# Kernel optimization log

Measured on AMD Instinct MI355X. Metric: run time of the kernel, lower is better.

The kernel has to match this reference:

```python
import jax, jax.numpy as jnp
import numpy as np

V, H, L, BW = 32000, 512, 2, 5   # vocab, hidden(=embed), gru layers, beam width
NEG = -1e9                        # -inf surrogate for duplicate initial beams


def gru_cell(x, h, Wi, Wh, bi, bh):
    # PyTorch GRU gate order: r, z, n.  x:[B,H] h:[B,H] Wi,Wh:[3H,H]
    gi = x @ Wi.T + bi
    gh = h @ Wh.T + bh
    ir, iz, inn = jnp.split(gi, 3, axis=-1)
    hr, hz, hn = jnp.split(gh, 3, axis=-1)
    r = jax.nn.sigmoid(ir + hr)
    z = jax.nn.sigmoid(iz + hz)
    n = jnp.tanh(inn + r * hn)
    return (1.0 - z) * n + z * h


def setup_inputs() -> dict:
    key = jax.random.key(0)
    ks = jax.random.split(key, 14)
    s = 0.05
    p = lambda k, shape: jax.random.normal(k, shape, jnp.float32) * s
    return {
        "input_seq": jax.random.randint(ks[0], (128, 1), 0, V),
        "input_length": 128,
        "max_length": 64,
        "SOS_token": 1,
        "emb": p(ks[1], (V, H)),
        "enc_Wi": p(ks[2], (L, 3 * H, H)),
        "enc_Wh": p(ks[3], (L, 3 * H, H)),
        "enc_bi": p(ks[4], (L, 3 * H)),
        "enc_bh": p(ks[5], (L, 3 * H)),
        "dec_Wi": p(ks[6], (L, 3 * H, H)),
        "dec_Wh": p(ks[7], (L, 3 * H, H)),
        "dec_bi": p(ks[8], (L, 3 * H)),
        "dec_bh": p(ks[9], (L, 3 * H)),
        "Wc": p(ks[10], (H, 2 * H)),
        "bc": p(ks[11], (H,)),
        "Wout": p(ks[12], (V, H)),
        "bout": p(ks[13], (V,)),
    }


def reference(input_seq, input_length, max_length, SOS_token,
              emb, enc_Wi, enc_Wh, enc_bi, enc_bh,
              dec_Wi, dec_Wh, dec_bi, dec_bh, Wc, bc, Wout, bout):
    # ---- encoder: L-layer GRU over [T,1] token ids ----
    x = emb[input_seq[:, 0]]                    # [T,H]

    def enc_step(h, xt):                        # h:[L,1,H]
        inp = xt[None]                          # [1,H]
        hs = []
        for l in range(L):
            hl = gru_cell(inp, h[l], enc_Wi[l], enc_Wh[l], enc_bi[l], enc_bh[l])
            hs.append(hl)
            inp = hl
        return jnp.stack(hs), inp[0]

    h0 = jnp.zeros((L, 1, H), x.dtype)
    enc_hidden, enc_out = jax.lax.scan(enc_step, h0, x)   # enc_out:[T,H]

    # ---- one decoder step, batched over all BW beams ----
    def dec_step(tokens, hidden):               # tokens:[BW] hidden:[L,BW,H]
        inp = emb[tokens]                       # [BW,H]
        hs = []
        for l in range(L):
            hl = gru_cell(inp, hidden[l], dec_Wi[l], dec_Wh[l], dec_bi[l], dec_bh[l])
            hs.append(hl)
            inp = hl
        rnn = inp                               # [BW,H] top-layer output
        e = jnp.einsum('bh,th->bt', rnn, enc_out)          # Luong dot scores
        a = jax.nn.softmax(e, axis=-1)
        ctx = a @ enc_out                       # [BW,H]
        cc = jnp.tanh(jnp.concatenate([rnn, ctx], axis=-1) @ Wc.T + bc)
        logits = cc @ Wout.T + bout             # [BW,V]
        return logits, jnp.stack(hs)

    # ---- beam search: all beams in one batched decoder call per step ----
    tokens0 = jnp.full((BW,), SOS_token, jnp.int32)
    hid0 = jnp.broadcast_to(enc_hidden, (L, BW, H))
    scores0 = jnp.full((BW,), NEG, jnp.float32).at[0].set(0.0)  # one live beam

    def step(carry, _):
        tokens, hidden, scores = carry
        logits, hidden = dec_step(tokens, hidden)
        logp = jax.nn.log_softmax(logits, axis=-1)
        top_lp, top_idx = jax.lax.top_k(logp, BW)            # [BW,BW]
        cand = (scores[:, None] + top_lp).reshape(-1)        # [BW*BW]
        sc, flat = jax.lax.top_k(cand, BW)
        parent = flat // BW
        new_tok = top_idx.reshape(-1)[flat]
        hidden = hidden[:, parent, :]
        return (new_tok, hidden, sc), (new_tok, parent)

    (_, _, final_scores), (toks, pars) = jax.lax.scan(
        step, (tokens0, hid0, scores0), None, length=max_length)

    # ---- backtrack best hypothesis through parent pointers ----
    best = jnp.argmax(final_scores)

    def back(beam, tp):
        t, p = tp
        return p[beam], t[beam]

    _, seq = jax.lax.scan(back, best, (toks, pars), reverse=True)
    return seq, final_scores[best]
```

## Files before the change

kernel.cpp:

```cpp
#include <hip/hip_runtime.h>
#include <math.h>

#define VV 32000
#define HH 512
#define G3 1536
#define TI 128
#define TO 64
#define NB 5
#define NEGF (-1000000000.0f)
#define NTHR 256
#define NT5 512
#define LSTR 32

struct Params {
  const int* seq;
  const int* sosp;
  const float *emb, *eWi, *eWh, *ebi, *ebh;
  const float *dWi, *dWh, *dbi, *dbh;
  const float *Wc, *bc, *Wout, *bout;
  unsigned* bar;
  int *cur_tok, *toks, *pars, *ptop_i;
  float *gi0, *eout, *h0b, *h1b, *dch, *cc, *ptop_v, *psum, *scores;
  float* out;
};

__device__ __forceinline__ float cldf(const float* p) {
  return __hip_atomic_load(p, __ATOMIC_RELAXED, __HIP_MEMORY_SCOPE_AGENT);
}
__device__ __forceinline__ void cstf(float* p, float v) {
  __hip_atomic_store(p, v, __ATOMIC_RELAXED, __HIP_MEMORY_SCOPE_AGENT);
}
__device__ __forceinline__ int cldi(const int* p) {
  return __hip_atomic_load(p, __ATOMIC_RELAXED, __HIP_MEMORY_SCOPE_AGENT);
}
__device__ __forceinline__ void csti(int* p, int v) {
  __hip_atomic_store(p, v, __ATOMIC_RELAXED, __HIP_MEMORY_SCOPE_AGENT);
}
__device__ __forceinline__ unsigned rldu(const unsigned* p) {
  return __hip_atomic_load(p, __ATOMIC_RELAXED, __HIP_MEMORY_SCOPE_AGENT);
}
typedef unsigned long long u64t;
union F2U { u64t u; float f[2]; };
__device__ __forceinline__ void cld2(float* d, const float* p) {
  F2U x; x.u = __hip_atomic_load((const u64t*)p, __ATOMIC_RELAXED, __HIP_MEMORY_SCOPE_AGENT);
  d[0] = x.f[0]; d[1] = x.f[1];
}

__device__ __forceinline__ void bar_arrive(unsigned* lines, int myline) {
  __syncthreads();
  if (threadIdx.x == 0)
    __hip_atomic_fetch_add(lines + myline * LSTR, 1u,
                           __ATOMIC_RELAXED, __HIP_MEMORY_SCOPE_AGENT);
}
template <int SLP>
__device__ __forceinline__ void bar_wait8(const unsigned* lines, unsigned tgt) {
  if (threadIdx.x < 64) {
    for (;;) {
      unsigned v = tgt;
      if (threadIdx.x < 8) v = rldu(lines + threadIdx.x * LSTR);
      if (__all(v >= tgt)) break;
      __builtin_amdgcn_s_sleep(SLP);
    }
  }
  __syncthreads();
}
__device__ __forceinline__ void bcast_store(unsigned* L, int NL, unsigned tok) {
  asm volatile("s_waitcnt vmcnt(0)" ::: "memory");
  for (int i = 0; i < NL; i++)
    __hip_atomic_store(L + i * LSTR, tok, __ATOMIC_RELAXED, __HIP_MEMORY_SCOPE_AGENT);
}
template <int SLP>
__device__ __forceinline__ void leaf_wait(const unsigned* L, int grp, unsigned tok) {
  if (threadIdx.x == 0) {
    while (rldu(L + grp * LSTR) < tok) __builtin_amdgcn_s_sleep(SLP);
  }
  __syncthreads();
}

__device__ __forceinline__ float wredf(float v) {
#pragma unroll
  for (int o = 32; o; o >>= 1) v += __shfl_xor(v, o, 64);
  return v;
}

__global__ void __launch_bounds__(NTHR) k_e0(Params p) {
  const int wg = blockIdx.x, tid = threadIdx.x;
  const int lane = tid & 63, wv = tid >> 6;
  if (wg == 0) {
    for (int i = tid; i < 2 * HH; i += NTHR) { cstf(&p.h0b[i], 0.f); cstf(&p.h1b[i], 0.f); }
  }
  for (int lr = 0; lr < 6; lr++) {
    int row = wg * 6 + lr;
    const float* W = p.eWi + (size_t)row * HH;
    float w0[8];
#pragma unroll
    for (int j = 0; j < 8; j++) w0[j] = W[j * 64 + lane];
    float bi = p.ebi[row];
    for (int t = wv; t < TI; t += 4) {
      const float* x = p.emb + (size_t)p.seq[t] * HH;
      float s = 0.f;
#pragma unroll
      for (int j = 0; j < 8; j++) s += w0[j] * x[j * 64 + lane];
      s = wredf(s);
      if (lane == 0) p.gi0[(size_t)t * G3 + row] = s + bi;
    }
  }
}

__device__ void enc_step(const Params& p, int T, int wg, int lane, int wv) {
  const int sIn = T & 1, sOut = sIn ^ 1;
  if (wv < 2) {
    if (T < TI) {
      float hv[8];
#pragma unroll
      for (int j = 0; j < 8; j++) hv[j] = cldf(&p.h0b[sIn * HH + j * 64 + lane]);
#pragma unroll
      for (int uu = 0; uu < 4; uu++) {
        int u = wg * 8 + wv * 4 + uu;
        float g[3];
#pragma unroll
        for (int gg = 0; gg < 3; gg++) {
          const float* W = p.eWh + (size_t)(gg * HH + u) * HH;
          float s = 0.f;
#pragma unroll
          for (int j = 0; j < 8; j++) s += W[j * 64 + lane] * hv[j];
          g[gg] = wredf(s);
        }
        if (lane == 0) {
          const float* gr = p.gi0 + (size_t)T * G3;
          float ir = gr[u], iz = gr[HH + u], inn = gr[2 * HH + u];
          float hr = g[0] + p.ebh[u], hz = g[1] + p.ebh[HH + u], hn = g[2] + p.ebh[2 * HH + u];
          float r = 1.f / (1.f + expf(-(ir + hr)));
          float z = 1.f / (1.f + expf(-(iz + hz)));
          float n = tanhf(inn + r * hn);
          float hp = cldf(&p.h0b[sIn * HH + u]);
          cstf(&p.h0b[sOut * HH + u], (1.f - z) * n + z * hp);
        }
      }
    }
  } else {
    if (T >= 1) {
      float xv[8], hv[8];
#pragma unroll
      for (int j = 0; j < 8; j++) {
        xv[j] = cldf(&p.h0b[sIn * HH + j * 64 + lane]);
        hv[j] = cldf(&p.h1b[sOut * HH + j * 64 + lane]);
      }
#pragma unroll
      for (int uu = 0; uu < 4; uu++) {
        int u = wg * 8 + (wv - 2) * 4 + uu;
        float gi[3], gh[3];
#pragma unroll
        for (int gg = 0; gg < 3; gg++) {
          const float* Wi1 = p.eWi + (size_t)G3 * HH + (size_t)(gg * HH + u) * HH;
          const float* Wh1 = p.eWh + (size_t)G3 * HH + (size_t)(gg * HH + u) * HH;
          float si = 0.f, s2 = 0.f;
#pragma unroll
          for (int j = 0; j < 8; j++) { si += Wi1[j * 64 + lane] * xv[j]; s2 += Wh1[j * 64 + lane] * hv[j]; }
          gi[gg] = wredf(si);
          gh[gg] = wredf(s2);
        }
        if (lane == 0) {
          const float* bi = p.ebi + G3;
          const float* bh = p.ebh + G3;
          float ir = gi[0] + bi[u], iz = gi[1] + bi[HH + u], inn = gi[2] + bi[2 * HH + u];
          float hr = gh[0] + bh[u], hz = gh[1] + bh[HH + u], hn = gh[2] + bh[2 * HH + u];
          float r = 1.f / (1.f + expf(-(ir + hr)));
          float z = 1.f / (1.f + expf(-(iz + hz)));
          float n = tanhf(inn + r * hn);
          float hp = cldf(&p.h1b[sOut * HH + u]);
          float hnew = (1.f - z) * n + z * hp;
          cstf(&p.h1b[sIn * HH + u], hnew);
          p.eout[(size_t)(T - 1) * HH + u] = hnew;
        }
      }
    }
  }
}

__global__ void __launch_bounds__(NTHR) k_e1x2(Params p, int k) {
  const int wg = blockIdx.x, tid = threadIdx.x;
  const int lane = tid & 63, wv = tid >> 6;
  unsigned* ceA = p.bar + 0 * LSTR;
  enc_step(p, 2 * k, wg, lane, wv);
  if (2 * k + 1 <= TI) {
    bar_arrive(ceA, wg & 7);
    bar_wait8<2>(ceA, (unsigned)(8 * (k + 1)));
    enc_step(p, 2 * k + 1, wg, lane, wv);
  }
}

__global__ void __launch_bounds__(NTHR) k_d0(Params p) {
  const int wg = blockIdx.x, tid = threadIdx.x;
  for (int i = tid + wg * NTHR; i < 2 * NB * HH; i += 64 * NTHR) {
    int l = i / (NB * HH);
    int rem = i - l * (NB * HH);
    int u = rem % HH;
    p.dch[(size_t)l * NB * HH + rem] = (l == 0) ? cldf(&p.h0b[u]) : cldf(&p.h1b[u]);
  }
  if (wg == 0 && tid < NB) {
    p.cur_tok[tid] = p.sosp[0];
    p.scores[tid] = (tid == 0) ? 0.f : NEGF;
  }
}

template <int LAYER>
__device__ void gru_body(const Params& p, float* sm, int t, int ib, int ob,
                         int wg, int tid, int lane, int wv) {
  float* sx = sm;
  float* sh = sm + NB * HH;
  float* fres = sm + 2 * NB * HH;
  int ct[NB], pr[NB];
#pragma unroll
  for (int b = 0; b < NB; b++) {
    ct[b] = (LAYER == 0) ? cldi(&p.cur_tok[b]) : 0;
    pr[b] = (t == 0) ? b : cldi(&p.pars[(t - 1) * NB + b]);
  }
  for (int i = tid; i < NB * (HH / 2); i += NTHR) {
    int b = i >> 8, c = (i & 255) << 1;
    float x2[2], h2[2];
    if (LAYER == 0) {
      const float* e = p.emb + (size_t)ct[b] * HH + c;
      x2[0] = e[0]; x2[1] = e[1];
    } else {
      cld2(x2, &p.dch[((size_t)(ob * 2 + 0) * NB + b) * HH + c]);
    }
    cld2(h2, &p.dch[((size_t)(ib * 2 + LAYER) * NB + pr[b]) * HH + c]);
    sx[b * HH + c] = x2[0]; sx[b * HH + c + 1] = x2[1];
    sh[b * HH + c] = h2[0]; sh[b * HH + c + 1] = h2[1];
  }
  __syncthreads();
  const float* Wi = p.dWi + (size_t)LAYER * G3 * HH;
  const float* Wh = p.dWh + (size_t)LAYER * G3 * HH;
#pragma unroll
  for (int k = 0; k < 12; k++) {
    const int m_ = k % 6;
    const int f = wv * 12 + k;
    const int ul = f / 6;
    const int u = wg * 8 + ul;
    const float* W = (m_ >= 3 ? Wh : Wi) + (size_t)((m_ % 3) * HH + u) * HH;
    const float* vecb = (m_ >= 3) ? sh : sx;
    float wd[8];
#pragma unroll
    for (int j = 0; j < 8; j++) wd[j] = W[j * 64 + lane];
    float a0 = 0.f, a1 = 0.f, a2 = 0.f, a3 = 0.f, a4 = 0.f;
#pragma unroll
    for (int j = 0; j < 8; j++) {
      float wj = wd[j];
      int o = j * 64 + lane;
      a0 += wj * vecb[0 * HH + o];
      a1 += wj * vecb[1 * HH + o];
      a2 += wj * vecb[2 * HH + o];
      a3 += wj * vecb[3 * HH + o];
      a4 += wj * vecb[4 * HH + o];
    }
    float r0 = wredf(a0), r1 = wredf(a1), r2 = wredf(a2), r3 = wredf(a3), r4 = wredf(a4);
    if (lane == 0) {
      fres[f * NB + 0] = r0; fres[f * NB + 1] = r1; fres[f * NB + 2] = r2;
      fres[f * NB + 3] = r3; fres[f * NB + 4] = r4;
    }
  }
  __syncthreads();
  if (tid < 8 * NB) {
    int ul = tid / NB, b = tid - ul * NB;
    int u = wg * 8 + ul;
    const float* bi = p.dbi + LAYER * G3;
    const float* bh = p.dbh + LAYER * G3;
    float ir = fres[(ul * 6 + 0) * NB + b] + bi[u];
    float iz = fres[(ul * 6 + 1) * NB + b] + bi[HH + u];
    float inn = fres[(ul * 6 + 2) * NB + b] + bi[2 * HH + u];
    float hr = fres[(ul * 6 + 3) * NB + b] + bh[u];
    float hz = fres[(ul * 6 + 4) * NB + b] + bh[HH + u];
    float hn = fres[(ul * 6 + 5) * NB + b] + bh[2 * HH + u];
    float hp = sh[b * HH + u];
    float r = 1.f / (1.f + expf(-(ir + hr)));
    float z = 1.f / (1.f + expf(-(iz + hz)));
    float n = tanhf(inn + r * hn);
    cstf(&p.dch[((size_t)(ob * 2 + LAYER) * NB + b) * HH + u], (1.f - z) * n + z * hp);
  }
  __syncthreads();
}

__global__ void __launch_bounds__(NTHR) k_gru2(Params p, int t) {
  const int wg = blockIdx.x, tid = threadIdx.x;
  const int lane = tid & 63, wv = tid >> 6;
  const int ib = t & 1, ob = ib ^ 1;
  __shared__ float sm[2 * NB * HH + 48 * NB];
  unsigned* gruA = p.bar + 8 * LSTR;
  gru_body<0>(p, sm, t, ib, ob, wg, tid, lane, wv);
  bar_arrive(gruA, wg & 7);
  bar_wait8<2>(gruA, (unsigned)(8 * (t + 1)));
  gru_body<1>(p, sm, t, ib, ob, wg, tid, lane, wv);
}

__global__ void __launch_bounds__(NT5) k_pa56(Params p, int t) {
  const int wg = blockIdx.x, tid = threadIdx.x;
  const int lane = tid & 63, wv = tid >> 6;
  const int ob = (t & 1) ^ 1;
  __shared__ float sm[5760];
  __shared__ unsigned s_mrg;
  unsigned* paA = p.bar + 16 * LSTR;
  unsigned* paF = p.bar + 24 * LSTR;
  unsigned* paL = p.bar + 32 * LSTR;
  unsigned* c5A = p.bar + 48 * LSTR;
  unsigned* c5F = p.bar + 56 * LSTR;

  if (wg < 40) {
    const int b = wg / 8, q = wg % 8;
    float* srnn = sm;
    float* sp = sm + 512;
    float* cpart = sm + 640;
    float* sctx = sm + 4736;
    for (int i = tid; i < HH; i += NT5)
      srnn[i] = cldf(&p.dch[((size_t)(ob * 2 + 1) * NB + b) * HH + i]);
    __syncthreads();
    for (int j = wv; j < TI; j += 8) {
      const float* E = p.eout + (size_t)j * HH;
      float s = 0.f;
#pragma unroll
      for (int k2 = 0; k2 < 8; k2++) s += srnn[k2 * 64 + lane] * E[k2 * 64 + lane];
      s = wredf(s);
      if (lane == 0) sp[j] = s;
    }
    __syncthreads();
    if (wv == 0) {
      float v0 = sp[lane], v1 = sp[64 + lane];
      float mx = fmaxf(v0, v1);
#pragma unroll
      for (int o = 32; o; o >>= 1) mx = fmaxf(mx, __shfl_xor(mx, o, 64));
      float e0 = expf(v0 - mx), e1 = expf(v1 - mx);
      float ss = wredf(e0 + e1);
      sp[lane] = e0 / ss;
      sp[64 + lane] = e1 / ss;
    }
    __syncthreads();
    {
      float cp[8];
#pragma unroll
      for (int k2 = 0; k2 < 8; k2++) cp[k2] = 0.f;
      for (int j = wv; j < TI; j += 8) {
        float spj = sp[j];
        const float* E = p.eout + (size_t)j * HH;
#pragma unroll
        for (int k2 = 0; k2 < 8; k2++) cp[k2] += spj * E[k2 * 64 + lane];
      }
#pragma unroll
      for (int k2 = 0; k2 < 8; k2++) cpart[wv * HH + k2 * 64 + lane] = cp[k2];
    }
    __syncthreads();
    for (int i = tid; i < HH; i += NT5)
      sctx[i] = ((cpart[0 * HH + i] + cpart[1 * HH + i]) + (cpart[2 * HH + i] + cpart[3 * HH + i]))
              + ((cpart[4 * HH + i] + cpart[5 * HH + i]) + (cpart[6 * HH + i] + cpart[7 * HH + i]));
    __syncthreads();
    for (int k = wv; k < 64; k += 8) {
      int u = q * 64 + k;
      const float* W = p.Wc + (size_t)u * (2 * HH);
      float s0 = 0.f, s1 = 0.f;
#pragma unroll
      for (int j = 0; j < 8; j++) {
        int o = j * 64 + lane;
        s0 += W[o] * srnn[o];
        s1 += W[HH + o] * sctx[o];
      }
      float r0 = wredf(s0), r1 = wredf(s1);
      if (lane == 0) cstf(&p.cc[b * HH + u], tanhf(r0 + r1 + p.bc[u]));
    }
    __syncthreads();
    if (tid == 0) {
      unsigned o1 = __hip_atomic_fetch_add(paA + (wg & 7) * LSTR, 1u,
                                           __ATOMIC_RELAXED, __HIP_MEMORY_SCOPE_AGENT);
      if (o1 == (unsigned)(5 * (t + 1) - 1)) {
        unsigned o2 = __hip_atomic_fetch_add(paF, 1u,
                                             __ATOMIC_RELAXED, __HIP_MEMORY_SCOPE_AGENT);
        if (o2 == (unsigned)(8 * (t + 1) - 1))
          bcast_store(paL, 16, (unsigned)(t + 1));
      }
    }
  }
  leaf_wait<4>(paL, wg >> 4, (unsigned)(t + 1));

  {
    float* scc = sm;
    float* slg = sm + 2560;
    float* part = sm + 3200;
    for (int i = tid; i < NB * (HH / 2); i += NT5) {
      int b = i >> 8, c = (i & 255) << 1;
      float c2v[2];
      cld2(c2v, &p.cc[b * HH + c]);
      scc[b * HH + c] = c2v[0]; scc[b * HH + c + 1] = c2v[1];
    }
    __syncthreads();
    const int vbase = wg * 125;
    if (tid < 500) {
      const int q = tid / 125, r = tid - q * 125;
      const float4* Wr = (const float4*)(p.Wout + (size_t)(vbase + r) * HH + q * 128);
      const float* sc0 = scc + q * 128;
      float a0 = 0.f, a1 = 0.f, a2 = 0.f, a3 = 0.f, a4 = 0.f;
#pragma unroll 8
      for (int c = 0; c < 32; c++) {
        float4 w = Wr[c];
        const float4 s0 = *(const float4*)(sc0 + 0 * HH + 4 * c);
        const float4 s1 = *(const float4*)(sc0 + 1 * HH + 4 * c);
        const float4 s2 = *(const float4*)(sc0 + 2 * HH + 4 * c);
        const float4 s3 = *(const float4*)(sc0 + 3 * HH + 4 * c);
        const float4 s4 = *(const float4*)(sc0 + 4 * HH + 4 * c);
        a0 += ((w.x * s0.x + w.y * s0.y) + (w.z * s0.z + w.w * s0.w));
        a1 += ((w.x * s1.x + w.y * s1.y) + (w.z * s1.z + w.w * s1.w));
        a2 += ((w.x * s2.x + w.y * s2.y) + (w.z * s2.z + w.w * s2.w));
        a3 += ((w.x * s3.x + w.y * s3.y) + (w.z * s3.z + w.w * s3.w));
        a4 += ((w.x * s4.x + w.y * s4.y) + (w.z * s4.z + w.w * s4.w));
      }
      float* pt = part + (size_t)tid * NB;
      pt[0] = a0; pt[1] = a1; pt[2] = a2; pt[3] = a3; pt[4] = a4;
    }
    __syncthreads();
    if (tid < 125) {
      float bo = p.bout[vbase + tid];
      const float* p0 = part + (size_t)(0 * 125 + tid) * NB;
      const float* p1 = part + (size_t)(1 * 125 + tid) * NB;
      const float* p2 = part + (size_t)(2 * 125 + tid) * NB;
      const float* p3 = part + (size_t)(3 * 125 + tid) * NB;
#pragma unroll
      for (int b = 0; b < NB; b++)
        slg[b * 125 + tid] = ((p0[b] + p1[b]) + (p2[b] + p3[b])) + bo;
    }
    __syncthreads();
    if (wv == 0) {
      for (int b = 0; b < NB; b++) {
        float s0 = (lane < 125) ? expf(slg[b * 125 + lane]) : 0.f;
        float s1 = (lane + 64 < 125) ? expf(slg[b * 125 + lane + 64]) : 0.f;
        float ss = wredf(s0 + s1);
        if (lane == 0) cstf(&p.psum[wg * NB + b], ss);
      }
    } else if (wv == 1 && lane < NB) {
      int b = lane;
      float bv[5]; int bidx[5];
#pragma unroll
      for (int k = 0; k < 5; k++) { bv[k] = -INFINITY; bidx[k] = 0x7fffffff; }
      for (int r = 0; r < 125; r++) {
        float v = slg[b * 125 + r];
        if (v > bv[4]) {
          int k = 4;
          while (k > 0 && v > bv[k - 1]) { bv[k] = bv[k - 1]; bidx[k] = bidx[k - 1]; k--; }
          bv[k] = v; bidx[k] = vbase + r;
        }
      }
#pragma unroll
      for (int k = 0; k < 5; k++) {
        cstf(&p.ptop_v[(wg * NB + b) * 5 + k], bv[k]);
        csti(&p.ptop_i[(wg * NB + b) * 5 + k], bidx[k]);
      }
    }
  }

  __syncthreads();
  if (tid == 0) {
    unsigned m = 0;
    unsigned o1 = __hip_atomic_fetch_add(c5A + (wg & 7) * LSTR, 1u,
                                         __ATOMIC_RELAXED, __HIP_MEMORY_SCOPE_AGENT);
    if (o1 == (unsigned)(32 * (t + 1) - 1)) {
      unsigned o2 = __hip_atomic_fetch_add(c5F, 1u,
                                           __ATOMIC_RELAXED, __HIP_MEMORY_SCOPE_AGENT);
      if (o2 == (unsigned)(8 * (t + 1) - 1)) m = 1;
    }
    s_mrg = m;
  }
  __syncthreads();

  if (s_mrg) {
    float* sls = sm;
    float* smv = sm + 8;
    int* smi = (int*)(sm + 40);
    for (int b = wv; b < NB; b += 8) {
      float q0 = cldf(&p.psum[(lane + 0) * NB + b]);
      float q1 = cldf(&p.psum[(lane + 64) * NB + b]);
      float q2 = cldf(&p.psum[(lane + 128) * NB + b]);
      float q3 = cldf(&p.psum[(lane + 192) * NB + b]);
      float ssum = wredf((q0 + q1) + (q2 + q3));
      float bv[5]; int bix[5];
#pragma unroll
      for (int k = 0; k < 5; k++) { bv[k] = -INFINITY; bix[k] = 0x7fffffff; }
      for (int g = 0; g < 4; g++) {
        int w = lane + g * 64;
#pragma unroll
        for (int k = 0; k < 5; k++) {
          float v = cldf(&p.ptop_v[((size_t)w * NB + b) * 5 + k]);
          int id = cldi(&p.ptop_i[((size_t)w * NB + b) * 5 + k]);
          if (v > bv[4] || (v == bv[4] && id < bix[4])) {
            int kk = 4;
            while (kk > 0 && (v > bv[kk - 1] || (v == bv[kk - 1] && id < bix[kk - 1]))) {
              bv[kk] = bv[kk - 1]; bix[kk] = bix[kk - 1]; kk--;
            }
            bv[kk] = v; bix[kk] = id;
          }
        }
      }
#pragma unroll
      for (int off = 1; off < 64; off <<= 1) {
        float ov[5]; int oi[5];
#pragma unroll
        for (int k = 0; k < 5; k++) { ov[k] = __shfl_xor(bv[k], off, 64); oi[k] = __shfl_xor(bix[k], off, 64); }
        float nv[5]; int ni[5];
        int i2 = 0, j2 = 0;
#pragma unroll
        for (int k = 0; k < 5; k++) {
          bool ta = (bv[i2] > ov[j2]) || (bv[i2] == ov[j2] && bix[i2] < oi[j2]);
          if (ta) { nv[k] = bv[i2]; ni[k] = bix[i2]; i2++; }
          else { nv[k] = ov[j2]; ni[k] = oi[j2]; j2++; }
        }
#pragma unroll
        for (int k = 0; k < 5; k++) { bv[k] = nv[k]; bix[k] = ni[k]; }
      }
      if (lane == 0) {
        sls[b] = logf(ssum);
#pragma unroll
        for (int k = 0; k < 5; k++) { smv[b * 5 + k] = bv[k]; smi[b * 5 + k] = bix[k]; }
      }
    }
    __syncthreads();
    if (tid == 0) {
      float cand[25]; int ctok[25];
      for (int b = 0; b < NB; b++) {
        float sb = cldf(&p.scores[b]), lb = sls[b];
#pragma unroll
        for (int k = 0; k < 5; k++) {
          cand[b * 5 + k] = sb + (smv[b * 5 + k] - lb);
          ctok[b * 5 + k] = smi[b * 5 + k];
        }
      }
      float s5[5]; int f5[5];
#pragma unroll
      for (int k = 0; k < 5; k++) { s5[k] = -INFINITY; f5[k] = 0x7fffffff; }
      for (int f = 0; f < 25; f++) {
        float v = cand[f];
        if (v > s5[4]) {
          int k = 4;
          while (k > 0 && v > s5[k - 1]) { s5[k] = s5[k - 1]; f5[k] = f5[k - 1]; k--; }
          s5[k] = v; f5[k] = f;
        }
      }
      for (int j2 = 0; j2 < 5; j2++) {
        int fl = f5[j2];
        csti(&p.pars[t * NB + j2], fl / 5);
        csti(&p.toks[t * NB + j2], ctok[fl]);
        csti(&p.cur_tok[j2], ctok[fl]);
      }
      for (int j2 = 0; j2 < 5; j2++) cstf(&p.scores[j2], s5[j2]);
      if (t == TO - 1) {
        int best = 0;
        float bvv = s5[0];
        for (int j = 1; j < NB; j++)
          if (s5[j] > bvv) { bvv = s5[j]; best = j; }
        int beam = best;
        for (int tt = TO - 1; tt >= 0; tt--) {
          p.out[tt] = (float)cldi(&p.toks[tt * NB + beam]);
          beam = cldi(&p.pars[tt * NB + beam]);
        }
        p.out[TO] = bvv;
      }
    }
  }
}

extern "C" void kernel_launch(void* const* d_in, const int* in_sizes, int n_in,
                              void* d_out, int out_size, void* d_ws, size_t ws_size,
                              hipStream_t stream) {
  (void)in_sizes; (void)n_in; (void)out_size; (void)ws_size;
  Params p;
  p.seq  = (const int*)d_in[0];
  p.sosp = (const int*)d_in[3];
  p.emb  = (const float*)d_in[4];
  p.eWi  = (const float*)d_in[5];
  p.eWh  = (const float*)d_in[6];
  p.ebi  = (const float*)d_in[7];
  p.ebh  = (const float*)d_in[8];
  p.dWi  = (const float*)d_in[9];
  p.dWh  = (const float*)d_in[10];
  p.dbi  = (const float*)d_in[11];
  p.dbh  = (const float*)d_in[12];
  p.Wc   = (const float*)d_in[13];
  p.bc   = (const float*)d_in[14];
  p.Wout = (const float*)d_in[15];
  p.bout = (const float*)d_in[16];

  char* w = (char*)d_ws;
  size_t off = 0;
  auto alloc = [&](size_t words) -> char* {
    char* r = w + off;
    off += words * 4;
    off = (off + 255) & ~(size_t)255;
    return r;
  };
  p.bar     = (unsigned*)alloc(64 * LSTR);
  p.cur_tok = (int*)alloc(8);
  p.toks    = (int*)alloc(TO * NB);
  p.pars    = (int*)alloc(TO * NB);
  p.ptop_i  = (int*)alloc(256 * NB * 5);
  p.gi0     = (float*)alloc((size_t)TI * G3);
  p.eout    = (float*)alloc((size_t)TI * HH);
  p.h0b     = (float*)alloc(2 * HH);
  p.h1b     = (float*)alloc(2 * HH);
  p.dch     = (float*)alloc(2 * 2 * NB * HH);
  p.cc      = (float*)alloc(NB * HH);
  p.ptop_v  = (float*)alloc(256 * NB * 5);
  p.psum    = (float*)alloc(256 * NB);
  p.scores  = (float*)alloc(8);
  p.out     = (float*)d_out;

  (void)hipMemsetAsync(d_ws, 0, 64 * LSTR * 4, stream);

  k_e0<<<dim3(256), dim3(NTHR), 0, stream>>>(p);
  for (int k = 0; k <= TI / 2; k++)
    k_e1x2<<<dim3(64), dim3(NTHR), 0, stream>>>(p, k);
  k_d0<<<dim3(64), dim3(NTHR), 0, stream>>>(p);
  for (int t = 0; t < TO; t++) {
    k_gru2<<<dim3(64), dim3(NTHR), 0, stream>>>(p, t);
    k_pa56<<<dim3(256), dim3(NT5), 0, stream>>>(p, t);
  }
}
```

Before: 7.022 ms.

## Split output projection across 500 workgroups with 64 vocab rows each

Measured after the change: 7.197 ms. 2.5% more time.

```diff
diff --git a/kernel.cpp b/kernel.cpp
--- a/kernel.cpp
+++ b/kernel.cpp
@@ -10,6 +10,7 @@
 #define NEGF (-1000000000.0f)
 #define NTHR 256
 #define NT5 512
+#define NCH 500
 #define LSTR 32
 
 struct Params {
@@ -301,9 +302,9 @@
   __shared__ unsigned s_mrg;
   unsigned* paA = p.bar + 16 * LSTR;
   unsigned* paF = p.bar + 24 * LSTR;
-  unsigned* paL = p.bar + 32 * LSTR;
   unsigned* c5A = p.bar + 48 * LSTR;
   unsigned* c5F = p.bar + 56 * LSTR;
+  unsigned* paL = p.bar + 64 * LSTR;
 
   if (wg < 40) {
     const int b = wg / 8, q = wg % 8;
@@ -373,7 +374,7 @@
         unsigned o2 = __hip_atomic_fetch_add(paF, 1u,
                                              __ATOMIC_RELAXED, __HIP_MEMORY_SCOPE_AGENT);
         if (o2 == (unsigned)(8 * (t + 1) - 1))
-          bcast_store(paL, 16, (unsigned)(t + 1));
+          bcast_store(paL, 32, (unsigned)(t + 1));
       }
     }
   }
@@ -382,7 +383,7 @@
   {
     float* scc = sm;
     float* slg = sm + 2560;
-    float* part = sm + 3200;
+    float* part = sm + 2944;
     for (int i = tid; i < NB * (HH / 2); i += NT5) {
       int b = i >> 8, c = (i & 255) << 1;
       float c2v[2];
@@ -390,14 +391,14 @@
       scc[b * HH + c] = c2v[0]; scc[b * HH + c + 1] = c2v[1];
     }
     __syncthreads();
-    const int vbase = wg * 125;
-    if (tid < 500) {
-      const int q = tid / 125, r = tid - q * 125;
-      const float4* Wr = (const float4*)(p.Wout + (size_t)(vbase + r) * HH + q * 128);
-      const float* sc0 = scc + q * 128;
+    const int vbase = wg * 64;
+    {
+      const int e = tid >> 6, r = tid & 63;
+      const float4* Wr = (const float4*)(p.Wout + (size_t)(vbase + r) * HH + e * 64);
+      const float* sc0 = scc + e * 64;
       float a0 = 0.f, a1 = 0.f, a2 = 0.f, a3 = 0.f, a4 = 0.f;
-#pragma unroll 8
-      for (int c = 0; c < 32; c++) {
+#pragma unroll
+      for (int c = 0; c < 16; c++) {
         float4 w = Wr[c];
         const float4 s0 = *(const float4*)(sc0 + 0 * HH + 4 * c);
         const float4 s1 = *(const float4*)(sc0 + 1 * HH + 4 * c);
@@ -414,22 +415,22 @@
       pt[0] = a0; pt[1] = a1; pt[2] = a2; pt[3] = a3; pt[4] = a4;
     }
     __syncthreads();
-    if (tid < 125) {
+    if (tid < 64) {
       float bo = p.bout[vbase + tid];
-      const float* p0 = part + (size_t)(0 * 125 + tid) * NB;
-      const float* p1 = part + (size_t)(1 * 125 + tid) * NB;
-      const float* p2 = part + (size_t)(2 * 125 + tid) * NB;
-      const float* p3 = part + (size_t)(3 * 125 + tid) * NB;
-#pragma unroll
-      for (int b = 0; b < NB; b++)
-        slg[b * 125 + tid] = ((p0[b] + p1[b]) + (p2[b] + p3[b])) + bo;
+#pragma unroll
+      for (int b = 0; b < NB; b++) {
+        float s01 = part[(size_t)(0 * 64 + tid) * NB + b] + part[(size_t)(1 * 64 + tid) * NB + b];
+        float s23 = part[(size_t)(2 * 64 + tid) * NB + b] + part[(size_t)(3 * 64 + tid) * NB + b];
+        float s45 = part[(size_t)(4 * 64 + tid) * NB + b] + part[(size_t)(5 * 64 + tid) * NB + b];
+        float s67 = part[(size_t)(6 * 64 + tid) * NB + b] + part[(size_t)(7 * 64 + tid) * NB + b];
+        slg[b * 64 + tid] = ((s01 + s23) + (s45 + s67)) + bo;
+      }
     }
     __syncthreads();
     if (wv == 0) {
       for (int b = 0; b < NB; b++) {
-        float s0 = (lane < 125) ? expf(slg[b * 125 + lane]) : 0.f;
-        float s1 = (lane + 64 < 125) ? expf(slg[b * 125 + lane + 64]) : 0.f;
-        float ss = wredf(s0 + s1);
+        float s0 = expf(slg[b * 64 + lane]);
+        float ss = wredf(s0);
         if (lane == 0) cstf(&p.psum[wg * NB + b], ss);
       }
     } else if (wv == 1 && lane < NB) {
@@ -437,8 +438,8 @@
       float bv[5]; int bidx[5];
 #pragma unroll
       for (int k = 0; k < 5; k++) { bv[k] = -INFINITY; bidx[k] = 0x7fffffff; }
-      for (int r = 0; r < 125; r++) {
-        float v = slg[b * 125 + r];
+      for (int r = 0; r < 64; r++) {
+        float v = slg[b * 64 + r];
         if (v > bv[4]) {
           int k = 4;
           while (k > 0 && v > bv[k - 1]) { bv[k] = bv[k - 1]; bidx[k] = bidx[k - 1]; k--; }
@@ -456,9 +457,10 @@
   __syncthreads();
   if (tid == 0) {
     unsigned m = 0;
+    const unsigned cnt = ((wg & 7) < 4) ? 63u : 62u;
     unsigned o1 = __hip_atomic_fetch_add(c5A + (wg & 7) * LSTR, 1u,
                                          __ATOMIC_RELAXED, __HIP_MEMORY_SCOPE_AGENT);
-    if (o1 == (unsigned)(32 * (t + 1) - 1)) {
+    if (o1 == cnt * (unsigned)(t + 1) - 1u) {
       unsigned o2 = __hip_atomic_fetch_add(c5F, 1u,
                                            __ATOMIC_RELAXED, __HIP_MEMORY_SCOPE_AGENT);
       if (o2 == (unsigned)(8 * (t + 1) - 1)) m = 1;
@@ -472,26 +474,30 @@
     float* smv = sm + 8;
     int* smi = (int*)(sm + 40);
     for (int b = wv; b < NB; b += 8) {
-      float q0 = cldf(&p.psum[(lane + 0) * NB + b]);
-      float q1 = cldf(&p.psum[(lane + 64) * NB + b]);
-      float q2 = cldf(&p.psum[(lane + 128) * NB + b]);
-      float q3 = cldf(&p.psum[(lane + 192) * NB + b]);
-      float ssum = wredf((q0 + q1) + (q2 + q3));
+      float qsum = 0.f;
+#pragma unroll
+      for (int g = 0; g < 8; g++) {
+        int w = lane + g * 64;
+        qsum += (w < NCH) ? cldf(&p.psum[(size_t)w * NB + b]) : 0.f;
+      }
+      float ssum = wredf(qsum);
       float bv[5]; int bix[5];
 #pragma unroll
       for (int k = 0; k < 5; k++) { bv[k] = -INFINITY; bix[k] = 0x7fffffff; }
-      for (int g = 0; g < 4; g++) {
+      for (int g = 0; g < 8; g++) {
         int w = lane + g * 64;
-#pragma unroll
-        for (int k = 0; k < 5; k++) {
-          float v = cldf(&p.ptop_v[((size_t)w * NB + b) * 5 + k]);
-          int id = cldi(&p.ptop_i[((size_t)w * NB + b) * 5 + k]);
-          if (v > bv[4] || (v == bv[4] && id < bix[4])) {
-            int kk = 4;
-            while (kk > 0 && (v > bv[kk - 1] || (v == bv[kk - 1] && id < bix[kk - 1]))) {
-              bv[kk] = bv[kk - 1]; bix[kk] = bix[kk - 1]; kk--;
+        if (w < NCH) {
+#pragma unroll
+          for (int k = 0; k < 5; k++) {
+            float v = cldf(&p.ptop_v[((size_t)w * NB + b) * 5 + k]);
+            int id = cldi(&p.ptop_i[((size_t)w * NB + b) * 5 + k]);
+            if (v > bv[4] || (v == bv[4] && id < bix[4])) {
+              int kk = 4;
+              while (kk > 0 && (v > bv[kk - 1] || (v == bv[kk - 1] && id < bix[kk - 1]))) {
+                bv[kk] = bv[kk - 1]; bix[kk] = bix[kk - 1]; kk--;
+              }
+              bv[kk] = v; bix[kk] = id;
             }
-            bv[kk] = v; bix[kk] = id;
           }
         }
       }
@@ -591,23 +597,23 @@
     off = (off + 255) & ~(size_t)255;
     return r;
   };
-  p.bar     = (unsigned*)alloc(64 * LSTR);
+  p.bar     = (unsigned*)alloc(96 * LSTR);
   p.cur_tok = (int*)alloc(8);
   p.toks    = (int*)alloc(TO * NB);
   p.pars    = (int*)alloc(TO * NB);
-  p.ptop_i  = (int*)alloc(256 * NB * 5);
+  p.ptop_i  = (int*)alloc(NCH * NB * 5);
   p.gi0     = (float*)alloc((size_t)TI * G3);
   p.eout    = (float*)alloc((size_t)TI * HH);
   p.h0b     = (float*)alloc(2 * HH);
   p.h1b     = (float*)alloc(2 * HH);
   p.dch     = (float*)alloc(2 * 2 * NB * HH);
   p.cc      = (float*)alloc(NB * HH);
-  p.ptop_v  = (float*)alloc(256 * NB * 5);
-  p.psum    = (float*)alloc(256 * NB);
+  p.ptop_v  = (float*)alloc(NCH * NB * 5);
+  p.psum    = (float*)alloc(NCH * NB);
   p.scores  = (float*)alloc(8);
   p.out     = (float*)d_out;
 
-  (void)hipMemsetAsync(d_ws, 0, 64 * LSTR * 4, stream);
+  (void)hipMemsetAsync(d_ws, 0, 96 * LSTR * 4, stream);
 
   k_e0<<<dim3(256), dim3(NTHR), 0, stream>>>(p);
   for (int k = 0; k <= TI / 2; k++)
@@ -615,6 +621,6 @@
   k_d0<<<dim3(64), dim3(NTHR), 0, stream>>>(p);
   for (int t = 0; t < TO; t++) {
     k_gru2<<<dim3(64), dim3(NTHR), 0, stream>>>(p, t);
-    k_pa56<<<dim3(256), dim3(NT5), 0, stream>>>(p, t);
-  }
-}
+    k_pa56<<<dim3(NCH), dim3(NT5), 0, stream>>>(p, t);
+  }
+}
```
